# Kernel tuning notes

Measured on AMD Instinct MI355X. Metric: run time of the kernel, lower is better.

Reference implementation:

```python
import jax, jax.numpy as jnp
import numpy as np

INTRA_K = 16
OUTER_K = 16
MAX_PAIR = 1024


def _mahalanobis(x, cov_inv, mean):
    # x: (..., D) difference vectors; returns squared Mahalanobis-style form (...,)
    xc = x - mean
    return jnp.einsum('...i,ij,...j->...', xc, cov_inv, xc)


def setup_inputs() -> dict:
    key = jax.random.key(0)
    k1, k2, k3 = jax.random.split(key, 3)
    B, N, M = 4, 1024, 1024
    outputs = jax.random.normal(k1, (B, N, 9), dtype=jnp.float32)
    targets = jax.random.normal(k2, (B, M, 9), dtype=jnp.float32)
    mask = jax.random.randint(k3, (B, M), 0, 2).astype(bool)
    return {"outputs": outputs, "targets": targets, "mask": mask}


def reference(outputs, targets, mask):
    y_pred = outputs[:, :MAX_PAIR]                      # (B, N, 9)
    m = mask.astype(y_pred.dtype)                       # (B, M)
    cnt = m.sum()

    # mean / covariance over masked true grasps (equivalent to boolean-gather)
    mean = (targets * m[..., None]).sum((0, 1)) / cnt   # (9,)
    centered = (targets - mean) * m[..., None]          # masked rows contribute 0
    flat = centered.reshape(-1, 9)
    cov = flat.T @ flat / (cnt - 1.0)                   # (9, 9)
    cov_inv = jnp.linalg.pinv(cov)

    # intra loss: true-vs-pred pairwise distances, masked rows excluded
    diff = targets[:, :, None, :] - y_pred[:, None, :, :]   # (B, M, N, 9)
    d = _mahalanobis(diff, cov_inv, mean)                   # (B, M, N)
    neg_topk, _ = jax.lax.top_k(-d, INTRA_K)                # k smallest
    row_sum = (-neg_topk).sum(-1)                           # (B, M)
    intra_loss = (row_sum * m).sum() / cnt                  # mean over masked rows

    # outer loss: pred-vs-pred pairwise distances, no mask
    diff_r = y_pred[:, None, :, :] - y_pred[:, :, None, :]  # (B, N, N, 9); [b,i,j] = pred[b,j]-pred[b,i]
    d_r = _mahalanobis(diff_r, cov_inv, mean)               # (B, N, N)
    neg_tk, _ = jax.lax.top_k(-d_r, OUTER_K)
    outer_loss = (-neg_tk).mean()

    return intra_loss, intra_loss, outer_loss
```

## Files before the change

kernel.cpp:

```cpp
#include <hip/hip_runtime.h>
#include <math.h>

#define BB   4
#define MM   1024
#define NN   1024
#define DD   9
#define KSEL 16
#define NROW (BB * MM)
#define NSLOT (2 * NROW)

struct Ws {
  float yT[BB * DD * NN];
  float qy[BB * NN];
  float rowsum[NSLOT];
  float cnt;
  float mean[DD];
  float cinv[DD * DD];
  unsigned int ticket;
};

__global__ __launch_bounds__(512) void setup_kernel(
    const float* __restrict__ outputs, const float* __restrict__ targets,
    const int* __restrict__ mask, Ws* __restrict__ ws) {
  const int tid = threadIdx.x;
  __shared__ float part[8][55];
  __shared__ double Sd[55];
  __shared__ float Cs[DD * DD];

  float acc[55];
#pragma unroll
  for (int k = 0; k < 55; ++k) acc[k] = 0.f;
  {
    const float4* tp = (const float4*)targets + 18 * tid;
    float4 st4[18];
#pragma unroll
    for (int i = 0; i < 18; ++i) st4[i] = tp[i];
    const float* f = (const float*)st4;
    const int4 m0 = ((const int4*)mask)[2 * tid];
    const int4 m1 = ((const int4*)mask)[2 * tid + 1];
    const int mk[8] = {m0.x, m0.y, m0.z, m0.w, m1.x, m1.y, m1.z, m1.w};
#pragma unroll
    for (int rr = 0; rr < 8; ++rr) {
      if (mk[rr] != 0) {
        const float* t = f + rr * DD;
        acc[0] += 1.f;
#pragma unroll
        for (int k = 0; k < DD; ++k) acc[1 + k] += t[k];
        int u = 10;
#pragma unroll
        for (int p = 0; p < DD; ++p)
#pragma unroll
          for (int q = p; q < DD; ++q) acc[u++] += t[p] * t[q];
      }
    }
  }
#pragma unroll
  for (int k = 0; k < 55; ++k) {
    float v = acc[k];
#pragma unroll
    for (int off = 32; off > 0; off >>= 1) v += __shfl_down(v, off, 64);
    if ((tid & 63) == 0) part[tid >> 6][k] = v;
  }
  if (tid == 0) ws->ticket = 0u;
  __syncthreads();

  if (tid < 55) {
    double s = 0.0;
#pragma unroll
    for (int w = 0; w < 8; ++w) s += (double)part[w][tid];
    Sd[tid] = s;
  }
  __syncthreads();

  if (tid < 64) {
    const int lane = tid;
    const double cnt = Sd[0];
    const int p = (lane < DD) ? lane : 0;
    double row[2 * DD];
    {
      const double mu_p = Sd[1 + p] / cnt;
#pragma unroll
      for (int q = 0; q < DD; ++q) {
        const int pp = (p < q) ? p : q;
        const int qq = (p < q) ? q : p;
        const int idx = 10 + 9 * pp - (pp * (pp - 1)) / 2 + (qq - pp);
        row[q] = (Sd[idx] - cnt * mu_p * (Sd[1 + q] / cnt)) / (cnt - 1.0);
        row[DD + q] = (p == q) ? 1.0 : 0.0;
      }
    }
#pragma unroll
    for (int c = 0; c < DD; ++c) {
      const double diag = __shfl(row[c], c, 64);
      const double dinv = 1.0 / diag;
      if (lane == c) {
#pragma unroll
        for (int q = 0; q < 2 * DD; ++q) row[q] *= dinv;
      }
      const double f = (lane == c) ? 0.0 : row[c];
#pragma unroll
      for (int q = 0; q < 2 * DD; ++q) {
        const double pv = __shfl(row[q], c, 64);
        row[q] -= f * pv;
      }
    }
    if (lane < DD) {
#pragma unroll
      for (int q = 0; q < DD; ++q) {
        const float cf = (float)row[DD + q];
        Cs[lane * DD + q] = cf;
        ws->cinv[lane * DD + q] = cf;
      }
    }
    if (lane == 0) {
      ws->cnt = (float)cnt;
#pragma unroll
      for (int q = 0; q < DD; ++q) ws->mean[q] = (float)(Sd[1 + q] / cnt);
    }
  }
  __syncthreads();

  {
    const int j0 = tid * 8;
    const int b = j0 >> 10;
    const int jj = j0 & (NN - 1);
    float C[DD * DD];
#pragma unroll
    for (int k = 0; k < DD * DD; ++k) C[k] = Cs[k];
    const float4* op4 = (const float4*)outputs + 18 * tid;
    float4 so4[18];
#pragma unroll
    for (int i = 0; i < 18; ++i) so4[i] = op4[i];
    const float* f = (const float*)so4;
#pragma unroll
    for (int g = 0; g < 2; ++g) {
      float qv[4];
#pragma unroll
      for (int rr = 0; rr < 4; ++rr) {
        const float* y = f + (g * 4 + rr) * DD;
        float qq = 0.f;
#pragma unroll
        for (int p = 0; p < DD; ++p) {
          float s = 0.f;
#pragma unroll
          for (int t = 0; t < DD; ++t) s += C[p * DD + t] * y[t];
          qq += y[p] * s;
        }
        qv[rr] = qq;
      }
#pragma unroll
      for (int p = 0; p < DD; ++p) {
        float4 o;
        o.x = f[(g * 4 + 0) * DD + p];
        o.y = f[(g * 4 + 1) * DD + p];
        o.z = f[(g * 4 + 2) * DD + p];
        o.w = f[(g * 4 + 3) * DD + p];
        *(float4*)(&ws->yT[(b * DD + p) * NN + jj + g * 4]) = o;
      }
      *(float4*)(&ws->qy[b * NN + jj + g * 4]) =
          make_float4(qv[0], qv[1], qv[2], qv[3]);
    }
  }
}

__device__ __forceinline__ float top16_sum(float (&v)[16]) {
#pragma unroll
  for (int k = 2; k <= 16; k <<= 1) {
#pragma unroll
    for (int j = k >> 1; j > 0; j >>= 1) {
#pragma unroll
      for (int i = 0; i < 16; ++i) {
        const int l = i ^ j;
        if (l > i) {
          const bool up = ((i & k) == 0);
          const float lo = fminf(v[i], v[l]);
          const float hi = fmaxf(v[i], v[l]);
          v[i] = up ? lo : hi;
          v[l] = up ? hi : lo;
        }
      }
    }
  }
#pragma unroll
  for (int off = 1; off < 64; off <<= 1) {
    float pr[16];
#pragma unroll
    for (int i = 0; i < 16; ++i) pr[i] = __shfl_xor(v[i], off, 64);
#pragma unroll
    for (int i = 0; i < 16; ++i) v[i] = fminf(v[i], pr[15 - i]);
    if (off < 32) {
#pragma unroll
      for (int j = 8; j > 0; j >>= 1) {
#pragma unroll
        for (int i = 0; i < 16; ++i) {
          const int l = i ^ j;
          if (l > i) {
            const float lo = fminf(v[i], v[l]);
            const float hi = fmaxf(v[i], v[l]);
            v[i] = lo;
            v[l] = hi;
          }
        }
      }
    }
  }
  float total = v[0];
#pragma unroll
  for (int k = 1; k < 16; ++k) total += v[k];
  return total;
}

__global__ __launch_bounds__(256) void dist_kernel(
    const float* __restrict__ outputs, const float* __restrict__ targets,
    const int* __restrict__ mask, Ws* __restrict__ ws,
    float* __restrict__ out) {
  const int tid = threadIdx.x;
  const int wv = tid >> 6;
  const int lane = tid & 63;
  const int r = blockIdx.x * 4 + wv;
  const int b = r >> 10;
  const bool live = (mask[r] != 0);

  float wo[DD];
  float qa_o = 0.f;
  {
    float ao[DD];
#pragma unroll
    for (int k = 0; k < DD; ++k) ao[k] = outputs[r * DD + k] + ws->mean[k];
#pragma unroll
    for (int p = 0; p < DD; ++p) {
      float s = 0.f;
#pragma unroll
      for (int t = 0; t < DD; ++t) s += ws->cinv[p * DD + t] * ao[t];
      wo[p] = s;
      qa_o += ao[p] * s;
    }
  }
  float wi[DD];
  float qa_i = 0.f;
  if (live) {
    float ai[DD];
#pragma unroll
    for (int k = 0; k < DD; ++k) ai[k] = targets[r * DD + k] - ws->mean[k];
#pragma unroll
    for (int p = 0; p < DD; ++p) {
      float s = 0.f;
#pragma unroll
      for (int t = 0; t < DD; ++t) s += ws->cinv[p * DD + t] * ai[t];
      wi[p] = s;
      qa_i += ai[p] * s;
    }
  }

  float vi[16], vo[16];
#pragma unroll
  for (int k = 0; k < 16; ++k) {
    vi[k] = 0.f;
    vo[k] = 0.f;
  }
  const float* __restrict__ yTb = ws->yT + (size_t)b * DD * NN;
  if (live) {
#pragma unroll
    for (int p = 0; p < DD; ++p) {
      const float4* __restrict__ pl = (const float4*)(yTb + (size_t)p * NN);
#pragma unroll
      for (int c = 0; c < 4; ++c) {
        const float4 y4 = pl[c * 64 + lane];
        vi[c * 4 + 0] += wi[p] * y4.x;
        vi[c * 4 + 1] += wi[p] * y4.y;
        vi[c * 4 + 2] += wi[p] * y4.z;
        vi[c * 4 + 3] += wi[p] * y4.w;
        vo[c * 4 + 0] += wo[p] * y4.x;
        vo[c * 4 + 1] += wo[p] * y4.y;
        vo[c * 4 + 2] += wo[p] * y4.z;
        vo[c * 4 + 3] += wo[p] * y4.w;
      }
    }
  } else {
#pragma unroll
    for (int p = 0; p < DD; ++p) {
      const float4* __restrict__ pl = (const float4*)(yTb + (size_t)p * NN);
#pragma unroll
      for (int c = 0; c < 4; ++c) {
        const float4 y4 = pl[c * 64 + lane];
        vo[c * 4 + 0] += wo[p] * y4.x;
        vo[c * 4 + 1] += wo[p] * y4.y;
        vo[c * 4 + 2] += wo[p] * y4.z;
        vo[c * 4 + 3] += wo[p] * y4.w;
      }
    }
  }
  {
    const float4* __restrict__ q4 = (const float4*)(ws->qy + (size_t)b * NN);
#pragma unroll
    for (int c = 0; c < 4; ++c) {
      const float4 qv = q4[c * 64 + lane];
      vo[c * 4 + 0] = qa_o + qv.x - 2.f * vo[c * 4 + 0];
      vo[c * 4 + 1] = qa_o + qv.y - 2.f * vo[c * 4 + 1];
      vo[c * 4 + 2] = qa_o + qv.z - 2.f * vo[c * 4 + 2];
      vo[c * 4 + 3] = qa_o + qv.w - 2.f * vo[c * 4 + 3];
      if (live) {
        vi[c * 4 + 0] = qa_i + qv.x - 2.f * vi[c * 4 + 0];
        vi[c * 4 + 1] = qa_i + qv.y - 2.f * vi[c * 4 + 1];
        vi[c * 4 + 2] = qa_i + qv.z - 2.f * vi[c * 4 + 2];
        vi[c * 4 + 3] = qa_i + qv.w - 2.f * vi[c * 4 + 3];
      }
    }
  }

  float si = 0.f;
  if (live) si = top16_sum(vi);
  const float so = top16_sum(vo);
  if (lane == 0) {
    __hip_atomic_store(&ws->rowsum[r], si, __ATOMIC_RELAXED,
                       __HIP_MEMORY_SCOPE_AGENT);
    __hip_atomic_store(&ws->rowsum[NROW + r], so, __ATOMIC_RELAXED,
                       __HIP_MEMORY_SCOPE_AGENT);
  }

  __syncthreads();
  __shared__ int slast;
  if (tid == 0) {
    const unsigned int old = __hip_atomic_fetch_add(
        &ws->ticket, 1u, __ATOMIC_ACQ_REL, __HIP_MEMORY_SCOPE_AGENT);
    slast = (old == (unsigned int)(gridDim.x - 1)) ? 1 : 0;
  }
  __syncthreads();
  if (slast != 0) {
    double li = 0.0, lo = 0.0;
    for (int k = tid; k < NROW; k += 256) {
      li += (double)__hip_atomic_load(&ws->rowsum[k], __ATOMIC_RELAXED,
                                      __HIP_MEMORY_SCOPE_AGENT);
      lo += (double)__hip_atomic_load(&ws->rowsum[NROW + k], __ATOMIC_RELAXED,
                                      __HIP_MEMORY_SCOPE_AGENT);
    }
#pragma unroll
    for (int off = 32; off > 0; off >>= 1) {
      li += __shfl_down(li, off, 64);
      lo += __shfl_down(lo, off, 64);
    }
    __shared__ double lds_i[4], lds_o[4];
    if ((tid & 63) == 0) {
      lds_i[tid >> 6] = li;
      lds_o[tid >> 6] = lo;
    }
    __syncthreads();
    if (tid == 0) {
      const double sI = lds_i[0] + lds_i[1] + lds_i[2] + lds_i[3];
      const double sO = lds_o[0] + lds_o[1] + lds_o[2] + lds_o[3];
      const float intra = (float)(sI / (double)ws->cnt);
      const float outer = (float)(sO / (double)(NROW * KSEL));
      out[0] = intra;
      out[1] = intra;
      out[2] = outer;
    }
  }
}

extern "C" void kernel_launch(void* const* d_in, const int* in_sizes, int n_in,
                              void* d_out, int out_size, void* d_ws,
                              size_t ws_size, hipStream_t stream) {
  const float* outputs = (const float*)d_in[0];
  const float* targets = (const float*)d_in[1];
  const int* mask = (const int*)d_in[2];
  Ws* ws = (Ws*)d_ws;
  float* out = (float*)d_out;

  setup_kernel<<<1, 512, 0, stream>>>(outputs, targets, mask, ws);
  dist_kernel<<<NROW / 4, 256, 0, stream>>>(outputs, targets, mask, ws, out);
}
```

Baseline: 119.4 us.

## Split final reduction into separate kernel and share code path for top-k selection

Replaces the last-block atomic ticket with a separate single-block finalize kernel, so dist_kernel ends with plain stores. The intra and outer projections are now computed unconditionally and together, and the two top-16 sorts run through one non-unrolled loop to shrink code size and register pressure. The cost is an extra kernel launch, redundant work for masked rows, and a serialized loop instead of inlined sorts.

```diff
diff --git a/kernel.cpp b/kernel.cpp
--- a/kernel.cpp
+++ b/kernel.cpp
@@ -16,7 +16,6 @@
   float cnt;
   float mean[DD];
   float cinv[DD * DD];
-  unsigned int ticket;
 };
 
 __global__ __launch_bounds__(512) void setup_kernel(
@@ -61,7 +60,6 @@
     for (int off = 32; off > 0; off >>= 1) v += __shfl_down(v, off, 64);
     if ((tid & 63) == 0) part[tid >> 6][k] = v;
   }
-  if (tid == 0) ws->ticket = 0u;
   __syncthreads();
 
   if (tid < 55) {
@@ -162,57 +160,9 @@
   }
 }
 
-__device__ __forceinline__ float top16_sum(float (&v)[16]) {
-#pragma unroll
-  for (int k = 2; k <= 16; k <<= 1) {
-#pragma unroll
-    for (int j = k >> 1; j > 0; j >>= 1) {
-#pragma unroll
-      for (int i = 0; i < 16; ++i) {
-        const int l = i ^ j;
-        if (l > i) {
-          const bool up = ((i & k) == 0);
-          const float lo = fminf(v[i], v[l]);
-          const float hi = fmaxf(v[i], v[l]);
-          v[i] = up ? lo : hi;
-          v[l] = up ? hi : lo;
-        }
-      }
-    }
-  }
-#pragma unroll
-  for (int off = 1; off < 64; off <<= 1) {
-    float pr[16];
-#pragma unroll
-    for (int i = 0; i < 16; ++i) pr[i] = __shfl_xor(v[i], off, 64);
-#pragma unroll
-    for (int i = 0; i < 16; ++i) v[i] = fminf(v[i], pr[15 - i]);
-    if (off < 32) {
-#pragma unroll
-      for (int j = 8; j > 0; j >>= 1) {
-#pragma unroll
-        for (int i = 0; i < 16; ++i) {
-          const int l = i ^ j;
-          if (l > i) {
-            const float lo = fminf(v[i], v[l]);
-            const float hi = fmaxf(v[i], v[l]);
-            v[i] = lo;
-            v[l] = hi;
-          }
-        }
-      }
-    }
-  }
-  float total = v[0];
-#pragma unroll
-  for (int k = 1; k < 16; ++k) total += v[k];
-  return total;
-}
-
 __global__ __launch_bounds__(256) void dist_kernel(
     const float* __restrict__ outputs, const float* __restrict__ targets,
-    const int* __restrict__ mask, Ws* __restrict__ ws,
-    float* __restrict__ out) {
+    const int* __restrict__ mask, Ws* __restrict__ ws) {
   const int tid = threadIdx.x;
   const int wv = tid >> 6;
   const int lane = tid & 63;
@@ -220,34 +170,29 @@
   const int b = r >> 10;
   const bool live = (mask[r] != 0);
 
-  float wo[DD];
-  float qa_o = 0.f;
+  float wo[DD], wi[DD];
+  float qa_o = 0.f, qa_i = 0.f;
   {
-    float ao[DD];
-#pragma unroll
-    for (int k = 0; k < DD; ++k) ao[k] = outputs[r * DD + k] + ws->mean[k];
+    float ao[DD], ai[DD];
+#pragma unroll
+    for (int k = 0; k < DD; ++k) {
+      const float mk = ws->mean[k];
+      ao[k] = outputs[r * DD + k] + mk;
+      ai[k] = targets[r * DD + k] - mk;
+    }
 #pragma unroll
     for (int p = 0; p < DD; ++p) {
-      float s = 0.f;
-#pragma unroll
-      for (int t = 0; t < DD; ++t) s += ws->cinv[p * DD + t] * ao[t];
-      wo[p] = s;
-      qa_o += ao[p] * s;
-    }
-  }
-  float wi[DD];
-  float qa_i = 0.f;
-  if (live) {
-    float ai[DD];
-#pragma unroll
-    for (int k = 0; k < DD; ++k) ai[k] = targets[r * DD + k] - ws->mean[k];
-#pragma unroll
-    for (int p = 0; p < DD; ++p) {
-      float s = 0.f;
-#pragma unroll
-      for (int t = 0; t < DD; ++t) s += ws->cinv[p * DD + t] * ai[t];
-      wi[p] = s;
-      qa_i += ai[p] * s;
+      float so = 0.f, si = 0.f;
+#pragma unroll
+      for (int t = 0; t < DD; ++t) {
+        const float cv = ws->cinv[p * DD + t];
+        so += cv * ao[t];
+        si += cv * ai[t];
+      }
+      wo[p] = so;
+      qa_o += ao[p] * so;
+      wi[p] = si;
+      qa_i += ai[p] * si;
     }
   }
 
@@ -258,35 +203,20 @@
     vo[k] = 0.f;
   }
   const float* __restrict__ yTb = ws->yT + (size_t)b * DD * NN;
-  if (live) {
-#pragma unroll
-    for (int p = 0; p < DD; ++p) {
-      const float4* __restrict__ pl = (const float4*)(yTb + (size_t)p * NN);
-#pragma unroll
-      for (int c = 0; c < 4; ++c) {
-        const float4 y4 = pl[c * 64 + lane];
-        vi[c * 4 + 0] += wi[p] * y4.x;
-        vi[c * 4 + 1] += wi[p] * y4.y;
-        vi[c * 4 + 2] += wi[p] * y4.z;
-        vi[c * 4 + 3] += wi[p] * y4.w;
-        vo[c * 4 + 0] += wo[p] * y4.x;
-        vo[c * 4 + 1] += wo[p] * y4.y;
-        vo[c * 4 + 2] += wo[p] * y4.z;
-        vo[c * 4 + 3] += wo[p] * y4.w;
-      }
-    }
-  } else {
-#pragma unroll
-    for (int p = 0; p < DD; ++p) {
-      const float4* __restrict__ pl = (const float4*)(yTb + (size_t)p * NN);
-#pragma unroll
-      for (int c = 0; c < 4; ++c) {
-        const float4 y4 = pl[c * 64 + lane];
-        vo[c * 4 + 0] += wo[p] * y4.x;
-        vo[c * 4 + 1] += wo[p] * y4.y;
-        vo[c * 4 + 2] += wo[p] * y4.z;
-        vo[c * 4 + 3] += wo[p] * y4.w;
-      }
+#pragma unroll
+  for (int p = 0; p < DD; ++p) {
+    const float4* __restrict__ pl = (const float4*)(yTb + (size_t)p * NN);
+#pragma unroll
+    for (int c = 0; c < 4; ++c) {
+      const float4 y4 = pl[c * 64 + lane];
+      vi[c * 4 + 0] += wi[p] * y4.x;
+      vi[c * 4 + 1] += wi[p] * y4.y;
+      vi[c * 4 + 2] += wi[p] * y4.z;
+      vi[c * 4 + 3] += wi[p] * y4.w;
+      vo[c * 4 + 0] += wo[p] * y4.x;
+      vo[c * 4 + 1] += wo[p] * y4.y;
+      vo[c * 4 + 2] += wo[p] * y4.z;
+      vo[c * 4 + 3] += wo[p] * y4.w;
     }
   }
   {
@@ -294,65 +224,104 @@
 #pragma unroll
     for (int c = 0; c < 4; ++c) {
       const float4 qv = q4[c * 64 + lane];
+      vi[c * 4 + 0] = qa_i + qv.x - 2.f * vi[c * 4 + 0];
+      vi[c * 4 + 1] = qa_i + qv.y - 2.f * vi[c * 4 + 1];
+      vi[c * 4 + 2] = qa_i + qv.z - 2.f * vi[c * 4 + 2];
+      vi[c * 4 + 3] = qa_i + qv.w - 2.f * vi[c * 4 + 3];
       vo[c * 4 + 0] = qa_o + qv.x - 2.f * vo[c * 4 + 0];
       vo[c * 4 + 1] = qa_o + qv.y - 2.f * vo[c * 4 + 1];
       vo[c * 4 + 2] = qa_o + qv.z - 2.f * vo[c * 4 + 2];
       vo[c * 4 + 3] = qa_o + qv.w - 2.f * vo[c * 4 + 3];
-      if (live) {
-        vi[c * 4 + 0] = qa_i + qv.x - 2.f * vi[c * 4 + 0];
-        vi[c * 4 + 1] = qa_i + qv.y - 2.f * vi[c * 4 + 1];
-        vi[c * 4 + 2] = qa_i + qv.z - 2.f * vi[c * 4 + 2];
-        vi[c * 4 + 3] = qa_i + qv.w - 2.f * vi[c * 4 + 3];
-      }
-    }
-  }
-
-  float si = 0.f;
-  if (live) si = top16_sum(vi);
-  const float so = top16_sum(vo);
+    }
+  }
+
+  float si_sum = 0.f, so_sum = 0.f;
+#pragma unroll 1
+  for (int s = live ? 0 : 1; s < 2; ++s) {
+    float v[16];
+#pragma unroll
+    for (int i = 0; i < 16; ++i) v[i] = (s == 0) ? vi[i] : vo[i];
+
+#pragma unroll
+    for (int k = 2; k <= 16; k <<= 1) {
+#pragma unroll
+      for (int j = k >> 1; j > 0; j >>= 1) {
+#pragma unroll
+        for (int i = 0; i < 16; ++i) {
+          const int l = i ^ j;
+          if (l > i) {
+            const bool up = ((i & k) == 0);
+            const float lo = fminf(v[i], v[l]);
+            const float hi = fmaxf(v[i], v[l]);
+            v[i] = up ? lo : hi;
+            v[l] = up ? hi : lo;
+          }
+        }
+      }
+    }
+#pragma unroll
+    for (int off = 1; off < 64; off <<= 1) {
+      float pr[16];
+#pragma unroll
+      for (int i = 0; i < 16; ++i) pr[i] = __shfl_xor(v[i], off, 64);
+#pragma unroll
+      for (int i = 0; i < 16; ++i) v[i] = fminf(v[i], pr[15 - i]);
+      if (off < 32) {
+#pragma unroll
+        for (int j = 8; j > 0; j >>= 1) {
+#pragma unroll
+          for (int i = 0; i < 16; ++i) {
+            const int l = i ^ j;
+            if (l > i) {
+              const float lo = fminf(v[i], v[l]);
+              const float hi = fmaxf(v[i], v[l]);
+              v[i] = lo;
+              v[l] = hi;
+            }
+          }
+        }
+      }
+    }
+    float total = v[0];
+#pragma unroll
+    for (int k = 1; k < 16; ++k) total += v[k];
+    if (s == 0) si_sum = total;
+    else so_sum = total;
+  }
+
   if (lane == 0) {
-    __hip_atomic_store(&ws->rowsum[r], si, __ATOMIC_RELAXED,
-                       __HIP_MEMORY_SCOPE_AGENT);
-    __hip_atomic_store(&ws->rowsum[NROW + r], so, __ATOMIC_RELAXED,
-                       __HIP_MEMORY_SCOPE_AGENT);
-  }
-
+    ws->rowsum[r] = si_sum;
+    ws->rowsum[NROW + r] = so_sum;
+  }
+}
+
+__global__ __launch_bounds__(256) void finalize_kernel(
+    const Ws* __restrict__ ws, float* __restrict__ out) {
+  const int tid = threadIdx.x;
+  double li = 0.0, lo = 0.0;
+  for (int k = tid; k < NROW; k += 256) {
+    li += (double)ws->rowsum[k];
+    lo += (double)ws->rowsum[NROW + k];
+  }
+#pragma unroll
+  for (int off = 32; off > 0; off >>= 1) {
+    li += __shfl_down(li, off, 64);
+    lo += __shfl_down(lo, off, 64);
+  }
+  __shared__ double lds_i[4], lds_o[4];
+  if ((tid & 63) == 0) {
+    lds_i[tid >> 6] = li;
+    lds_o[tid >> 6] = lo;
+  }
   __syncthreads();
-  __shared__ int slast;
   if (tid == 0) {
-    const unsigned int old = __hip_atomic_fetch_add(
-        &ws->ticket, 1u, __ATOMIC_ACQ_REL, __HIP_MEMORY_SCOPE_AGENT);
-    slast = (old == (unsigned int)(gridDim.x - 1)) ? 1 : 0;
-  }
-  __syncthreads();
-  if (slast != 0) {
-    double li = 0.0, lo = 0.0;
-    for (int k = tid; k < NROW; k += 256) {
-      li += (double)__hip_atomic_load(&ws->rowsum[k], __ATOMIC_RELAXED,
-                                      __HIP_MEMORY_SCOPE_AGENT);
-      lo += (double)__hip_atomic_load(&ws->rowsum[NROW + k], __ATOMIC_RELAXED,
-                                      __HIP_MEMORY_SCOPE_AGENT);
-    }
-#pragma unroll
-    for (int off = 32; off > 0; off >>= 1) {
-      li += __shfl_down(li, off, 64);
-      lo += __shfl_down(lo, off, 64);
-    }
-    __shared__ double lds_i[4], lds_o[4];
-    if ((tid & 63) == 0) {
-      lds_i[tid >> 6] = li;
-      lds_o[tid >> 6] = lo;
-    }
-    __syncthreads();
-    if (tid == 0) {
-      const double sI = lds_i[0] + lds_i[1] + lds_i[2] + lds_i[3];
-      const double sO = lds_o[0] + lds_o[1] + lds_o[2] + lds_o[3];
-      const float intra = (float)(sI / (double)ws->cnt);
-      const float outer = (float)(sO / (double)(NROW * KSEL));
-      out[0] = intra;
-      out[1] = intra;
-      out[2] = outer;
-    }
+    const double sI = lds_i[0] + lds_i[1] + lds_i[2] + lds_i[3];
+    const double sO = lds_o[0] + lds_o[1] + lds_o[2] + lds_o[3];
+    const float intra = (float)(sI / (double)ws->cnt);
+    const float outer = (float)(sO / (double)(NROW * KSEL));
+    out[0] = intra;
+    out[1] = intra;
+    out[2] = outer;
   }
 }
 
@@ -366,5 +335,6 @@
   float* out = (float*)d_out;
 
   setup_kernel<<<1, 512, 0, stream>>>(outputs, targets, mask, ws);
-  dist_kernel<<<NROW / 4, 256, 0, stream>>>(outputs, targets, mask, ws, out);
+  dist_kernel<<<NROW / 4, 256, 0, stream>>>(outputs, targets, mask, ws);
+  finalize_kernel<<<1, 256, 0, stream>>>(ws, out);
 }
```

Measured after the change: 107.9 us. 1.11x faster.
